# Performance work log

Measured on AMD Instinct MI355X. Metric: run time of the kernel, lower is better.

Reference implementation:

```python
import jax, jax.numpy as jnp
import numpy as np

C, P, G = 80, 30000, 800       # classes, preds/class, gts/class
IOU_THR = 0.5
IMG = 1024.0                   # synthetic image size
BATCH = 16                     # images per batch (box[0] = image index)


def _make_boxes(key, n_cls, n):
    """Boxes in the module's 7-col layout: [img_idx, class, score, x1, y1, x2, y2]."""
    k1, k2, k3, k4 = jax.random.split(key, 4)
    xy = jax.random.uniform(k1, (n_cls, n, 2), minval=0.0, maxval=IMG - 128.0)
    wh = jax.random.uniform(k2, (n_cls, n, 2), minval=4.0, maxval=128.0)
    score = jax.random.uniform(k3, (n_cls, n, 1))
    img_idx = jax.random.randint(k4, (n_cls, n, 1), 0, BATCH).astype(jnp.float32)
    cls = jnp.zeros((n_cls, n, 1), jnp.float32)
    return jnp.concatenate([img_idx, cls, score, xy, xy + wh], axis=-1)


def setup_inputs() -> dict:
    key = jax.random.key(0)
    kp, kg = jax.random.split(key)
    return {"pred_boxes": _make_boxes(kp, C, P), "gt_boxes": _make_boxes(kg, C, G)}


def _pairwise_iou(a, b):
    # a: [P,4], b: [G,4] corner-format xyxy -> [P,G]
    lt = jnp.maximum(a[:, None, :2], b[None, :, :2])
    rb = jnp.minimum(a[:, None, 2:], b[None, :, 2:])
    wh = jnp.clip(rb - lt, 0.0)
    inter = wh[..., 0] * wh[..., 1]
    area_a = (a[:, 2] - a[:, 0]) * (a[:, 3] - a[:, 1])
    area_b = (b[:, 2] - b[:, 0]) * (b[:, 3] - b[:, 1])
    return inter / (area_a[:, None] + area_b[None, :] - inter + 1e-9)


def _ap_one_class(pb, gb):
    # pb: [P,7] preds, gb: [G,7] gts for one class
    n_p, n_g = pb.shape[0], gb.shape[0]
    order = jnp.argsort(-pb[:, 2])             # sort preds by score desc
    boxes = pb[order, 3:7]
    iou = _pairwise_iou(boxes, gb[:, 3:7])     # [P,G]
    best_iou = iou.max(axis=1)
    match = iou.argmax(axis=1)                 # best gt per pred
    valid = best_iou > IOU_THR
    p_idx = jnp.arange(n_p, dtype=jnp.int32)
    # first (highest-score) valid pred claiming each gt -> TP; later claims -> FP
    first = jnp.full((n_g,), n_p, jnp.int32).at[match].min(
        jnp.where(valid, p_idx, n_p))
    tp = (valid & (p_idx == first[match])).astype(jnp.float32)
    ctp = jnp.cumsum(tp)
    cfp = jnp.cumsum(1.0 - tp)
    recall = ctp / (n_g + 1e-9)
    precision = ctp / (ctp + cfp + 1e-9)
    # trapezoidal AP over the PR curve (torch.trapz(precisions, recalls))
    return jnp.sum((recall[1:] - recall[:-1]) * (precision[1:] + precision[:-1]) * 0.5)


def reference(pred_boxes, gt_boxes):
    # sequential map over classes keeps peak memory at one [P,G] IoU matrix
    aps = jax.lax.map(lambda ab: _ap_one_class(ab[0], ab[1]), (pred_boxes, gt_boxes))
    return jnp.mean(aps)
```

## Files before the change

### kernel.cpp

```cpp
#include <hip/hip_runtime.h>

#define C 80
#define P 30000
#define G 800
#define BS 256
#define NB 16
#define NC (NB * NB)
#define PPT 8
#define TPB (BS * PPT)
#define HCH 8
#define CHSZ ((P + HCH - 1) / HCH)


__device__ __forceinline__ unsigned long long pack_key(float s, int p) {
    return ((unsigned long long)__float_as_uint(s) << 32) | (unsigned)(P - 1 - p);
}

__device__ __forceinline__ int cell_of_center(float cxf, float cyf) {
    int bx = min(max((int)(cxf * (1.0f / 64.0f)), 0), NB - 1);
    int by = min(max((int)(cyf * (1.0f / 64.0f)), 0), NB - 1);
    return by * NB + bx;
}

__global__ __launch_bounds__(BS) void gt_bin_kernel(
        const float* __restrict__ gt,
        unsigned short* __restrict__ gtCnt, unsigned short* __restrict__ gtOff,
        float4* __restrict__ gtBox, float* __restrict__ gtAbe,
        unsigned short* __restrict__ gtIdx,
        unsigned long long* __restrict__ gtKey, int* __restrict__ gHist,
        unsigned int* __restrict__ doneCnt) {
    __shared__ int h[NC], cur[NC];
    __shared__ int gcell[G];
    const int c = blockIdx.x, tid = threadIdx.x;
    h[tid] = 0;
    if (c == 0 && tid == 0) *doneCnt = 0u;
    for (int i = tid; i < G; i += BS) gtKey[c * G + i] = 0ull;
    for (int j = tid; j < 1024; j += BS) gHist[c * 1024 + j] = 0;
    __syncthreads();
    for (int i = tid; i < G; i += BS) {
        const float* r = gt + ((size_t)c * G + i) * 7;
        int cl = cell_of_center(0.5f * (r[3] + r[5]), 0.5f * (r[4] + r[6]));
        gcell[i] = cl;
        atomicAdd(&h[cl], 1);
    }
    __syncthreads();
    const int v = h[tid];
    cur[tid] = v;
    __syncthreads();
    for (int o = 1; o < NC; o <<= 1) {
        int t = (tid >= o) ? cur[tid - o] : 0;
        __syncthreads();
        cur[tid] += t;
        __syncthreads();
    }
    const int excl = cur[tid] - v;
    gtOff[c * NC + tid] = (unsigned short)excl;
    gtCnt[c * NC + tid] = (unsigned short)v;
    __syncthreads();
    cur[tid] = excl;
    __syncthreads();
    for (int i = tid; i < G; i += BS) {
        const float* r = gt + ((size_t)c * G + i) * 7;
        float x1 = r[3], y1 = r[4], x2 = r[5], y2 = r[6];
        int slot = atomicAdd(&cur[gcell[i]], 1);
        gtBox[c * G + slot] = make_float4(x1, y1, x2, y2);
        gtAbe[c * G + slot] = __fadd_rn(__fmul_rn(__fsub_rn(x2, x1), __fsub_rn(y2, y1)), 1e-9f);
        gtIdx[c * G + slot] = (unsigned short)i;
    }
}

__global__ __launch_bounds__(BS) void match6_kernel(
        const float* __restrict__ pred,
        const unsigned short* __restrict__ gtOff, const unsigned short* __restrict__ gtCnt,
        const float4* __restrict__ gtBox, const float* __restrict__ gtAbe,
        const unsigned short* __restrict__ gtIdx,
        unsigned long long* __restrict__ gtKey) {
    __shared__ float sX1[G], sY1[G], sX2[G], sY2[G], sE[G];
    __shared__ unsigned short sG[G];
    __shared__ unsigned short sOff[NC], sCnt[NC];
    __shared__ unsigned char  sCell[TPB];
    __shared__ unsigned short sIdx[TPB];
    __shared__ int hcnt[NC], bb[NC];
    const int c = blockIdx.y, tid = threadIdx.x;
    const int p0 = blockIdx.x * TPB;
    const int cntP = min(TPB, P - p0);

    for (int i = tid; i < G; i += BS) {
        float4 b = gtBox[c * G + i];
        sX1[i] = b.x; sY1[i] = b.y; sX2[i] = b.z; sY2[i] = b.w;
        sE[i] = gtAbe[c * G + i];
        sG[i] = gtIdx[c * G + i];
    }
    sOff[tid] = gtOff[c * NC + tid];
    sCnt[tid] = gtCnt[c * NC + tid];
    hcnt[tid] = 0;
    __syncthreads();

    const size_t cp = (size_t)c * P;

    unsigned char  cellA[PPT];
    unsigned short lrA[PPT];
    #pragma unroll
    for (int rep = 0; rep < PPT; ++rep) {
        const int li = rep * BS + tid;
        const int p  = p0 + li;
        int cell = 0, lr = 0;
        if (p < P) {
            const float* r = pred + (cp + p) * 7;
            cell = cell_of_center(0.5f * (r[3] + r[5]), 0.5f * (r[4] + r[6]));
            lr = atomicAdd(&hcnt[cell], 1);
        }
        sCell[li] = (unsigned char)cell;
        cellA[rep] = (unsigned char)cell;
        lrA[rep] = (unsigned short)lr;
    }
    __syncthreads();

    const int v = hcnt[tid];
    __syncthreads();
    for (int o = 1; o < NC; o <<= 1) {
        int t = (tid >= o) ? hcnt[tid - o] : 0;
        __syncthreads();
        hcnt[tid] += t;
        __syncthreads();
    }
    bb[tid] = hcnt[tid] - v;
    __syncthreads();

    #pragma unroll
    for (int rep = 0; rep < PPT; ++rep) {
        const int li = rep * BS + tid;
        if (p0 + li < P) sIdx[bb[cellA[rep]] + lrA[rep]] = (unsigned short)li;
    }
    __syncthreads();

    #pragma unroll 1
    for (int rep = 0; rep < PPT; ++rep) {
        const int si = rep * BS + tid;
        if (si < cntP) {
            const int li = sIdx[si];
            const int p  = p0 + li;
            const float* r = pred + (cp + p) * 7;
            float ax1 = r[3], ay1 = r[4], ax2 = r[5], ay2 = r[6];
            float A = __fmul_rn(__fsub_rn(ax2, ax1), __fsub_rn(ay2, ay1));
            const int cell = sCell[li];
            const int cx = cell & (NB - 1), cy = cell >> 4;
            const int x0 = max(cx - 1, 0), x1 = min(cx + 1, NB - 1);
            const int y0 = max(cy - 1, 0), y1 = min(cy + 1, NB - 1);
            float IN = 0.0f, SB = 1.0f;
            int mj = -1;
            for (int yy = y0; yy <= y1; ++yy) {
                const int rowb = yy * NB;
                const int jb = sOff[rowb + x0];
                const int je = sOff[rowb + x1] + sCnt[rowb + x1];
                for (int j = jb; j < je; ++j) {
                    float bx1 = sX1[j], by1 = sY1[j];
                    float bx2 = sX2[j], by2 = sY2[j];
                    float lx = fmaxf(ax1, bx1), ly = fmaxf(ay1, by1);
                    float rx = fminf(ax2, bx2), ry = fminf(ay2, by2);
                    float wx = fmaxf(__fsub_rn(rx, lx), 0.0f);
                    float wy = fmaxf(__fsub_rn(ry, ly), 0.0f);
                    float in = __fmul_rn(wx, wy);
                    float sb = __fadd_rn(A, sE[j]);
                    bool  up = __fmul_rn(in, SB) > __fmul_rn(IN, sb);
                    IN = up ? in : IN; SB = up ? sb : SB; mj = up ? j : mj;
                }
            }
            if (IN > 0.0f) {
                float bx1 = sX1[mj], by1 = sY1[mj], bx2 = sX2[mj], by2 = sY2[mj];
                float area = __fmul_rn(__fsub_rn(bx2, bx1), __fsub_rn(by2, by1));
                float dn = __fadd_rn(__fsub_rn(__fadd_rn(A, area), IN), 1e-9f);
                float iou = __fdiv_rn(IN, dn);
                if (iou > 0.5f) {
                    float sscore = r[2];
                    atomicMax(&gtKey[c * G + sG[mj]], pack_key(sscore, p));
                }
            }
        }
    }
}

__global__ __launch_bounds__(BS) void sortc_kernel(
        const unsigned long long* __restrict__ gtKey,
        unsigned long long* __restrict__ sortedKeys, int* __restrict__ sortT) {
    __shared__ unsigned long long k[G];
    __shared__ unsigned long long sk[1024];
    __shared__ int cnt;
    const int c = blockIdx.x, tid = threadIdx.x;
    if (tid == 0) cnt = 0;
    for (int j = tid; j < 1024; j += BS) sk[j] = 0ull;
    __syncthreads();
    for (int i = tid; i < G; i += BS) {
        unsigned long long key = gtKey[c * G + i];
        if (key != 0ull) k[atomicAdd(&cnt, 1)] = key;
    }
    __syncthreads();
    const int T = cnt;
    if (tid == 0) sortT[c] = T;
    for (int t = tid; t < T; t += BS) {
        unsigned long long key = k[t];
        int pos = 0;
        for (int u = 0; u < T; ++u) pos += (k[u] > key) ? 1 : 0;
        sk[pos] = key;
    }
    __syncthreads();
    for (int j = tid; j < 1024; j += BS) sortedKeys[c * 1024 + j] = sk[j];
}

__global__ __launch_bounds__(BS) void hist_kernel(
        const float* __restrict__ pred,
        const unsigned long long* __restrict__ sortedKeys,
        int* __restrict__ gHist) {
    __shared__ unsigned long long sK[1024];
    __shared__ int h[1024];
    const int c = blockIdx.y, tid = threadIdx.x;
    for (int j = tid; j < 1024; j += BS) { sK[j] = sortedKeys[c * 1024 + j]; h[j] = 0; }
    __syncthreads();
    const int start = blockIdx.x * CHSZ;
    const int end   = min(start + CHSZ, P);
    const float* pr = pred + (size_t)c * P * 7;
    for (int i = start + tid; i < end; i += BS) {
        unsigned long long kq =
            ((unsigned long long)__float_as_uint(pr[(size_t)i * 7 + 2]) << 32)
            | (unsigned)(P - 1 - i);
        int lo = 0;
        #pragma unroll
        for (int step = 512; step > 0; step >>= 1)
            if (sK[lo + step - 1] > kq) lo += step;
        atomicAdd(&h[lo], 1);
    }
    __syncthreads();
    for (int j = tid; j < 1024; j += BS)
        if (h[j]) atomicAdd(&gHist[c * 1024 + j], h[j]);
}

__global__ __launch_bounds__(BS) void ap2m_kernel(
        const int* __restrict__ sortT, const int* __restrict__ gHist,
        float* __restrict__ ap, unsigned int* __restrict__ doneCnt,
        float* __restrict__ out) {
    __shared__ int ha[1024];
    __shared__ int hb[1024];
    __shared__ float red[BS];
    const int c = blockIdx.x, tid = threadIdx.x;
    const int T = sortT[c];
    for (int j = tid; j < 1024; j += BS) ha[j] = gHist[c * 1024 + j];
    __syncthreads();
    int* src = ha; int* dst = hb;
    for (int o = 1; o < 1024; o <<= 1) {
        for (int j = tid; j < 1024; j += BS)
            dst[j] = src[j] + ((j >= o) ? src[j - o] : 0);
        __syncthreads();
        int* tmp = src; src = dst; dst = tmp;
    }
    float sum = 0.0f;
    for (int s = tid; s < T; s += BS) {
        int r = src[s] - 1;
        if (r >= 1) {
            float kf  = (float)(s + 1);
            float km  = (float)s;
            float ri  = __fdiv_rn(kf, 800.0f);
            float rim = __fdiv_rn(km, 800.0f);
            float pi  = __fdiv_rn(kf, (float)(r + 1));
            float pim = __fdiv_rn(km, (float)r);
            sum = __fadd_rn(sum,
                  __fmul_rn(__fmul_rn(__fsub_rn(ri, rim), __fadd_rn(pi, pim)), 0.5f));
        }
    }
    red[tid] = sum;
    __syncthreads();
    for (int s2 = BS / 2; s2 > 0; s2 >>= 1) {
        if (tid < s2) red[tid] = __fadd_rn(red[tid], red[tid + s2]);
        __syncthreads();
    }
    if (tid == 0) {
        ap[c] = red[0];
        __threadfence();
        unsigned int t = atomicAdd(doneCnt, 1u);
        if (t == C - 1) {
            __threadfence();
            float s = 0.0f;
            for (int c2 = 0; c2 < C; ++c2) s = __fadd_rn(s, ap[c2]);
            out[0] = __fdiv_rn(s, 80.0f);
        }
    }
}

extern "C" void kernel_launch(void* const* d_in, const int* in_sizes, int n_in,
                              void* d_out, int out_size, void* d_ws, size_t ws_size,
                              hipStream_t stream) {
    const float* pred = (const float*)d_in[0];
    const float* gt   = (const float*)d_in[1];
    float* out = (float*)d_out;

    char* ws = (char*)d_ws;
    int*                sortT      = (int*)               (ws + 0);
    float*              ap         = (float*)             (ws + 512);
    unsigned int*       doneCnt    = (unsigned int*)      (ws + 896);
    unsigned short*     gtCnt      = (unsigned short*)    (ws + 1024);
    unsigned short*     gtOff      = (unsigned short*)    (ws + 41984);
    unsigned short*     gtIdx      = (unsigned short*)    (ws + 82944);
    float*              gtAbe      = (float*)             (ws + 210944);
    float4*             gtBox      = (float4*)            (ws + 466944);
    unsigned long long* gtKey      = (unsigned long long*)(ws + 1490944);
    unsigned long long* sortedKeys = (unsigned long long*)(ws + 2002944);
    int*                gHist      = (int*)               (ws + 2658304);

    const int M_BLK = (P + TPB - 1) / TPB;

    gt_bin_kernel<<<C, BS, 0, stream>>>(gt, gtCnt, gtOff, gtBox, gtAbe, gtIdx,
                                        gtKey, gHist, doneCnt);
    match6_kernel<<<dim3(M_BLK, C), BS, 0, stream>>>(pred, gtOff, gtCnt, gtBox,
                                                     gtAbe, gtIdx, gtKey);
    sortc_kernel<<<C, BS, 0, stream>>>(gtKey, sortedKeys, sortT);
    hist_kernel<<<dim3(HCH, C), BS, 0, stream>>>(pred, sortedKeys, gHist);
    ap2m_kernel<<<C, BS, 0, stream>>>(sortT, gHist, ap, doneCnt, out);
}
```

Measured before the change: 230.5 us.

## Fuse sort, histogram and AP kernels into one finale kernel; pack GT boxes as float4

Merges the three tail kernels (key sort, score histogram, AP integration) into a single per-class kernel, removing two launches and the global round trips for sorted keys and histograms. The histogram pass now runs with only 80 blocks (one per class) over all 30000 preds instead of 8 chunks per class, which reduces parallelism for that stage. The match kernel also stores GT boxes as float4 in shared memory, recomputes the cell instead of storing it, and unrolls the inner loop by 2.

```diff
diff --git a/kernel.cpp b/kernel.cpp
--- a/kernel.cpp
+++ b/kernel.cpp
@@ -8,8 +8,6 @@
 #define NC (NB * NB)
 #define PPT 8
 #define TPB (BS * PPT)
-#define HCH 8
-#define CHSZ ((P + HCH - 1) / HCH)
 
 
 __device__ __forceinline__ unsigned long long pack_key(float s, int p) {
@@ -27,7 +25,7 @@
         unsigned short* __restrict__ gtCnt, unsigned short* __restrict__ gtOff,
         float4* __restrict__ gtBox, float* __restrict__ gtAbe,
         unsigned short* __restrict__ gtIdx,
-        unsigned long long* __restrict__ gtKey, int* __restrict__ gHist,
+        unsigned long long* __restrict__ gtKey,
         unsigned int* __restrict__ doneCnt) {
     __shared__ int h[NC], cur[NC];
     __shared__ int gcell[G];
@@ -35,7 +33,6 @@
     h[tid] = 0;
     if (c == 0 && tid == 0) *doneCnt = 0u;
     for (int i = tid; i < G; i += BS) gtKey[c * G + i] = 0ull;
-    for (int j = tid; j < 1024; j += BS) gHist[c * 1024 + j] = 0;
     __syncthreads();
     for (int i = tid; i < G; i += BS) {
         const float* r = gt + ((size_t)c * G + i) * 7;
@@ -69,16 +66,16 @@
     }
 }
 
-__global__ __launch_bounds__(BS) void match6_kernel(
+__global__ __launch_bounds__(BS) void match7_kernel(
         const float* __restrict__ pred,
         const unsigned short* __restrict__ gtOff, const unsigned short* __restrict__ gtCnt,
         const float4* __restrict__ gtBox, const float* __restrict__ gtAbe,
         const unsigned short* __restrict__ gtIdx,
         unsigned long long* __restrict__ gtKey) {
-    __shared__ float sX1[G], sY1[G], sX2[G], sY2[G], sE[G];
+    __shared__ float4 sB[G];
+    __shared__ float  sE[G];
     __shared__ unsigned short sG[G];
     __shared__ unsigned short sOff[NC], sCnt[NC];
-    __shared__ unsigned char  sCell[TPB];
     __shared__ unsigned short sIdx[TPB];
     __shared__ int hcnt[NC], bb[NC];
     const int c = blockIdx.y, tid = threadIdx.x;
@@ -86,8 +83,7 @@
     const int cntP = min(TPB, P - p0);
 
     for (int i = tid; i < G; i += BS) {
-        float4 b = gtBox[c * G + i];
-        sX1[i] = b.x; sY1[i] = b.y; sX2[i] = b.z; sY2[i] = b.w;
+        sB[i] = gtBox[c * G + i];
         sE[i] = gtAbe[c * G + i];
         sG[i] = gtIdx[c * G + i];
     }
@@ -110,7 +106,6 @@
             cell = cell_of_center(0.5f * (r[3] + r[5]), 0.5f * (r[4] + r[6]));
             lr = atomicAdd(&hcnt[cell], 1);
         }
-        sCell[li] = (unsigned char)cell;
         cellA[rep] = (unsigned char)cell;
         lrA[rep] = (unsigned short)lr;
     }
@@ -143,7 +138,7 @@
             const float* r = pred + (cp + p) * 7;
             float ax1 = r[3], ay1 = r[4], ax2 = r[5], ay2 = r[6];
             float A = __fmul_rn(__fsub_rn(ax2, ax1), __fsub_rn(ay2, ay1));
-            const int cell = sCell[li];
+            const int cell = cell_of_center(0.5f * (ax1 + ax2), 0.5f * (ay1 + ay2));
             const int cx = cell & (NB - 1), cy = cell >> 4;
             const int x0 = max(cx - 1, 0), x1 = min(cx + 1, NB - 1);
             const int y0 = max(cy - 1, 0), y1 = min(cy + 1, NB - 1);
@@ -153,11 +148,11 @@
                 const int rowb = yy * NB;
                 const int jb = sOff[rowb + x0];
                 const int je = sOff[rowb + x1] + sCnt[rowb + x1];
+                #pragma unroll 2
                 for (int j = jb; j < je; ++j) {
-                    float bx1 = sX1[j], by1 = sY1[j];
-                    float bx2 = sX2[j], by2 = sY2[j];
-                    float lx = fmaxf(ax1, bx1), ly = fmaxf(ay1, by1);
-                    float rx = fminf(ax2, bx2), ry = fminf(ay2, by2);
+                    float4 b = sB[j];
+                    float lx = fmaxf(ax1, b.x), ly = fmaxf(ay1, b.y);
+                    float rx = fminf(ax2, b.z), ry = fminf(ay2, b.w);
                     float wx = fmaxf(__fsub_rn(rx, lx), 0.0f);
                     float wy = fmaxf(__fsub_rn(ry, ly), 0.0f);
                     float in = __fmul_rn(wx, wy);
@@ -167,8 +162,8 @@
                 }
             }
             if (IN > 0.0f) {
-                float bx1 = sX1[mj], by1 = sY1[mj], bx2 = sX2[mj], by2 = sY2[mj];
-                float area = __fmul_rn(__fsub_rn(bx2, bx1), __fsub_rn(by2, by1));
+                float4 b = sB[mj];
+                float area = __fmul_rn(__fsub_rn(b.z, b.x), __fsub_rn(b.w, b.y));
                 float dn = __fadd_rn(__fsub_rn(__fadd_rn(A, area), IN), 1e-9f);
                 float iou = __fdiv_rn(IN, dn);
                 if (iou > 0.5f) {
@@ -180,15 +175,21 @@
     }
 }
 
-__global__ __launch_bounds__(BS) void sortc_kernel(
+__global__ __launch_bounds__(BS) void finale_kernel(
+        const float* __restrict__ pred,
         const unsigned long long* __restrict__ gtKey,
-        unsigned long long* __restrict__ sortedKeys, int* __restrict__ sortT) {
+        float* __restrict__ ap, unsigned int* __restrict__ doneCnt,
+        float* __restrict__ out) {
     __shared__ unsigned long long k[G];
     __shared__ unsigned long long sk[1024];
+    __shared__ int h[1024];
+    __shared__ int hb[1024];
+    __shared__ float red[BS];
     __shared__ int cnt;
     const int c = blockIdx.x, tid = threadIdx.x;
+
     if (tid == 0) cnt = 0;
-    for (int j = tid; j < 1024; j += BS) sk[j] = 0ull;
+    for (int j = tid; j < 1024; j += BS) { sk[j] = 0ull; h[j] = 0; }
     __syncthreads();
     for (int i = tid; i < G; i += BS) {
         unsigned long long key = gtKey[c * G + i];
@@ -196,7 +197,7 @@
     }
     __syncthreads();
     const int T = cnt;
-    if (tid == 0) sortT[c] = T;
+
     for (int t = tid; t < T; t += BS) {
         unsigned long long key = k[t];
         int pos = 0;
@@ -204,54 +205,28 @@
         sk[pos] = key;
     }
     __syncthreads();
-    for (int j = tid; j < 1024; j += BS) sortedKeys[c * 1024 + j] = sk[j];
-}
-
-__global__ __launch_bounds__(BS) void hist_kernel(
-        const float* __restrict__ pred,
-        const unsigned long long* __restrict__ sortedKeys,
-        int* __restrict__ gHist) {
-    __shared__ unsigned long long sK[1024];
-    __shared__ int h[1024];
-    const int c = blockIdx.y, tid = threadIdx.x;
-    for (int j = tid; j < 1024; j += BS) { sK[j] = sortedKeys[c * 1024 + j]; h[j] = 0; }
-    __syncthreads();
-    const int start = blockIdx.x * CHSZ;
-    const int end   = min(start + CHSZ, P);
+
     const float* pr = pred + (size_t)c * P * 7;
-    for (int i = start + tid; i < end; i += BS) {
+    for (int i = tid; i < P; i += BS) {
         unsigned long long kq =
             ((unsigned long long)__float_as_uint(pr[(size_t)i * 7 + 2]) << 32)
             | (unsigned)(P - 1 - i);
         int lo = 0;
         #pragma unroll
         for (int step = 512; step > 0; step >>= 1)
-            if (sK[lo + step - 1] > kq) lo += step;
+            if (sk[lo + step - 1] > kq) lo += step;
         atomicAdd(&h[lo], 1);
     }
     __syncthreads();
-    for (int j = tid; j < 1024; j += BS)
-        if (h[j]) atomicAdd(&gHist[c * 1024 + j], h[j]);
-}
-
-__global__ __launch_bounds__(BS) void ap2m_kernel(
-        const int* __restrict__ sortT, const int* __restrict__ gHist,
-        float* __restrict__ ap, unsigned int* __restrict__ doneCnt,
-        float* __restrict__ out) {
-    __shared__ int ha[1024];
-    __shared__ int hb[1024];
-    __shared__ float red[BS];
-    const int c = blockIdx.x, tid = threadIdx.x;
-    const int T = sortT[c];
-    for (int j = tid; j < 1024; j += BS) ha[j] = gHist[c * 1024 + j];
-    __syncthreads();
-    int* src = ha; int* dst = hb;
+
+    int* src = h; int* dst = hb;
     for (int o = 1; o < 1024; o <<= 1) {
         for (int j = tid; j < 1024; j += BS)
             dst[j] = src[j] + ((j >= o) ? src[j - o] : 0);
         __syncthreads();
         int* tmp = src; src = dst; dst = tmp;
     }
+
     float sum = 0.0f;
     for (int s = tid; s < T; s += BS) {
         int r = src[s] - 1;
@@ -293,25 +268,20 @@
     float* out = (float*)d_out;
 
     char* ws = (char*)d_ws;
-    int*                sortT      = (int*)               (ws + 0);
-    float*              ap         = (float*)             (ws + 512);
-    unsigned int*       doneCnt    = (unsigned int*)      (ws + 896);
+    float*              ap         = (float*)             (ws + 0);
+    unsigned int*       doneCnt    = (unsigned int*)      (ws + 512);
     unsigned short*     gtCnt      = (unsigned short*)    (ws + 1024);
     unsigned short*     gtOff      = (unsigned short*)    (ws + 41984);
     unsigned short*     gtIdx      = (unsigned short*)    (ws + 82944);
     float*              gtAbe      = (float*)             (ws + 210944);
     float4*             gtBox      = (float4*)            (ws + 466944);
     unsigned long long* gtKey      = (unsigned long long*)(ws + 1490944);
-    unsigned long long* sortedKeys = (unsigned long long*)(ws + 2002944);
-    int*                gHist      = (int*)               (ws + 2658304);
 
     const int M_BLK = (P + TPB - 1) / TPB;
 
     gt_bin_kernel<<<C, BS, 0, stream>>>(gt, gtCnt, gtOff, gtBox, gtAbe, gtIdx,
-                                        gtKey, gHist, doneCnt);
-    match6_kernel<<<dim3(M_BLK, C), BS, 0, stream>>>(pred, gtOff, gtCnt, gtBox,
+                                        gtKey, doneCnt);
+    match7_kernel<<<dim3(M_BLK, C), BS, 0, stream>>>(pred, gtOff, gtCnt, gtBox,
                                                      gtAbe, gtIdx, gtKey);
-    sortc_kernel<<<C, BS, 0, stream>>>(gtKey, sortedKeys, sortT);
-    hist_kernel<<<dim3(HCH, C), BS, 0, stream>>>(pred, sortedKeys, gHist);
-    ap2m_kernel<<<C, BS, 0, stream>>>(sortT, gHist, ap, doneCnt, out);
-}
+    finale_kernel<<<C, BS, 0, stream>>>(pred, gtKey, ap, doneCnt, out);
+}
```

After: 280.4 us. 1.22x slower.
